# Kernel tuning notes

Measured on AMD Instinct MI355X. Metric: run time of the kernel, lower is better.

The kernel has to match this reference:

```python
import jax, jax.numpy as jnp
import numpy as np

B, T, Q, D = 8192, 65, 20, 100  # batch, tweet len, question len, 2*hidden_dim


def setup_inputs() -> dict:
    key = jax.random.key(0)
    kH, kU, k1, k2, k3 = jax.random.split(key, 5)
    # Ws params are a single normal row repeated across the length dim
    ws1 = jnp.tile(jax.random.normal(k1, (1, D), dtype=jnp.float32), (T, 1))
    ws2 = jnp.tile(jax.random.normal(k2, (1, D), dtype=jnp.float32), (Q, 1))
    ws3 = jnp.tile(jax.random.normal(k3, (1, D), dtype=jnp.float32), (T, 1))
    return {
        "H": jax.random.normal(kH, (B, T, D), dtype=jnp.float32),
        "U": jax.random.normal(kU, (B, Q, D), dtype=jnp.float32),
        "Ws1": ws1,
        "Ws2": ws2,
        "Ws3": ws3,
    }


def reference(H, U, Ws1, Ws2, Ws3):
    # H: [B,T,D], U: [B,Q,D]
    H1 = jnp.sum(H * Ws1, axis=2)[:, :, None]        # [B,T,1]
    U1 = jnp.sum(U * Ws2, axis=2)[:, None, :]        # [B,1,Q]
    HU = jnp.einsum('btd,bqd->btq', H * Ws3, U)      # [B,T,Q]
    S = H1 + U1 + HU                                 # [B,T,Q]
    at = jax.nn.softmax(S, axis=2)                   # attend tweet->question
    Util = jnp.einsum('btq,bqd->btd', at, U)         # [B,T,D]
    beta = jnp.max(S, axis=2)                        # [B,T]
    b = jax.nn.softmax(beta, axis=1)[:, :, None]     # [B,T,1]
    Htil = jnp.sum(b * H, axis=1)[:, None, :]        # [B,1,D] broadcast over T
    G = jnp.concatenate((H, Util, H * Util, H * Htil), axis=2)  # [B,T,4D]
    return G
```

## Files before the change

kernel.cpp:

```cpp
#include <hip/hip_runtime.h>
#include <math.h>

#define NB 8192
#define T 65
#define Q 20
#define D 100
#define D4 25
#define SP4 5

__global__ __launch_bounds__(256, 4) void attn_fused_kernel(
    const float* __restrict__ Hg,
    const float* __restrict__ Ug,
    const float* __restrict__ Ws1,
    const float* __restrict__ Ws2,
    const float* __restrict__ Ws3,
    float* __restrict__ Gg)
{
    __shared__ float4 sH4[T*D4];
    __shared__ float4 sU3e4[(Q+1)*D4];
    __shared__ float4 sS4[T*SP4];
    __shared__ float4 sHtilP[2][D4];
    __shared__ float4 sU1q4[5];
    __shared__ float  sScal[T];

    const int b    = blockIdx.x;
    const int tid  = threadIdx.x;
    const int wv   = tid >> 6;
    const int lane = tid & 63;
    const float4* Hb = (const float4*)(Hg + (size_t)b * (T*D));
    const float4* Ub = (const float4*)(Ug + (size_t)b * (Q*D));
    float* Gb = Gg + (size_t)b * (T*4*D);
    float4* Gb4 = (float4*)Gb;
    float* sSf = (float*)sS4;

    for (int i = tid; i < T*D4; i += 256) {
        const float4 h = Hb[i];
        sH4[i] = h;
        const int t = i / D4;
        const int g = i - t*D4;
        Gb4[t*100 + g] = h;
    }
    {
        const float4* w3g = (const float4*)Ws3;
        for (int i = tid; i < Q*D4; i += 256) {
            const float4 u = Ub[i];
            const int dd = i - (i/D4)*D4;
            const float4 w = w3g[dd];
            float4 v; v.x=u.x*w.x; v.y=u.y*w.y; v.z=u.z*w.z; v.w=u.w*w.w;
            sU3e4[i] = v;
        }
        if (tid < D4) sU3e4[Q*D4 + tid] = ((const float4*)Ws1)[tid];
    }
    __syncthreads();

    if (tid < 119) {
        const int tg = tid / 7;
        const int jg = tid - tg*7;
        int rb0 = ((tg*4 + 0) < T ? (tg*4 + 0) : T-1) * D4;
        int rb1 = ((tg*4 + 1) < T ? (tg*4 + 1) : T-1) * D4;
        int rb2 = ((tg*4 + 2) < T ? (tg*4 + 2) : T-1) * D4;
        int rb3 = ((tg*4 + 3) < T ? (tg*4 + 3) : T-1) * D4;
        float acc[4][3];
        #pragma unroll
        for (int i = 0; i < 4; ++i)
            #pragma unroll
            for (int k = 0; k < 3; ++k) acc[i][k] = 0.f;
        #pragma unroll 5
        for (int d4 = 0; d4 < D4; ++d4) {
            float4 h0 = sH4[rb0 + d4];
            float4 h1 = sH4[rb1 + d4];
            float4 h2 = sH4[rb2 + d4];
            float4 h3 = sH4[rb3 + d4];
            #pragma unroll
            for (int k = 0; k < 3; ++k) {
                const float4 w = sU3e4[(jg*3+k)*D4 + d4];
                acc[0][k] = fmaf(h0.x, w.x, acc[0][k]); acc[0][k] = fmaf(h0.y, w.y, acc[0][k]);
                acc[0][k] = fmaf(h0.z, w.z, acc[0][k]); acc[0][k] = fmaf(h0.w, w.w, acc[0][k]);
                acc[1][k] = fmaf(h1.x, w.x, acc[1][k]); acc[1][k] = fmaf(h1.y, w.y, acc[1][k]);
                acc[1][k] = fmaf(h1.z, w.z, acc[1][k]); acc[1][k] = fmaf(h1.w, w.w, acc[1][k]);
                acc[2][k] = fmaf(h2.x, w.x, acc[2][k]); acc[2][k] = fmaf(h2.y, w.y, acc[2][k]);
                acc[2][k] = fmaf(h2.z, w.z, acc[2][k]); acc[2][k] = fmaf(h2.w, w.w, acc[2][k]);
                acc[3][k] = fmaf(h3.x, w.x, acc[3][k]); acc[3][k] = fmaf(h3.y, w.y, acc[3][k]);
                acc[3][k] = fmaf(h3.z, w.z, acc[3][k]); acc[3][k] = fmaf(h3.w, w.w, acc[3][k]);
            }
        }
        #pragma unroll
        for (int i = 0; i < 4; ++i) {
            const int t = tg*4 + i;
            if (t < T) {
                #pragma unroll
                for (int k = 0; k < 3; ++k) {
                    const int cc = jg*3 + k;
                    if (cc < Q) sSf[t*Q + cc] = acc[i][k];
                    else        sScal[t] = acc[i][k];
                }
            }
        }
    } else if (tid >= 128 && tid < 128 + Q) {
        const int q = tid - 128;
        const float4* ur = Ub + q*D4;
        const float4* w2 = (const float4*)Ws2;
        float acc = 0.f;
        #pragma unroll 5
        for (int k = 0; k < D4; ++k) {
            const float4 u = ur[k], w = w2[k];
            acc = fmaf(u.x, w.x, acc); acc = fmaf(u.y, w.y, acc);
            acc = fmaf(u.z, w.z, acc); acc = fmaf(u.w, w.w, acc);
        }
        ((float*)sU1q4)[q] = acc;
    }
    __syncthreads();

    if (tid < T) {
        const int t = tid;
        float4 r[SP4];
        #pragma unroll
        for (int c = 0; c < SP4; ++c) {
            r[c] = sS4[t*SP4 + c];
            const float4 u1 = sU1q4[c];
            r[c].x += u1.x; r[c].y += u1.y; r[c].z += u1.z; r[c].w += u1.w;
        }
        float m = -1e30f;
        #pragma unroll
        for (int c = 0; c < SP4; ++c)
            m = fmaxf(m, fmaxf(fmaxf(r[c].x, r[c].y), fmaxf(r[c].z, r[c].w)));
        float s = 0.f;
        #pragma unroll
        for (int c = 0; c < SP4; ++c) {
            r[c].x = __expf(r[c].x - m); r[c].y = __expf(r[c].y - m);
            r[c].z = __expf(r[c].z - m); r[c].w = __expf(r[c].w - m);
            s += r[c].x + r[c].y + r[c].z + r[c].w;
        }
        const float inv = 1.f / s;
        #pragma unroll
        for (int c = 0; c < SP4; ++c) {
            r[c].x *= inv; r[c].y *= inv; r[c].z *= inv; r[c].w *= inv;
            sS4[t*SP4 + c] = r[c];
        }
        sScal[t] = sScal[t] + m;
    }
    __syncthreads();

    if (wv < 2) {
        const float v0 = sScal[lane];
        const float v1 = (lane == 0) ? sScal[64] : -1e30f;
        float mx = fmaxf(v0, v1);
        #pragma unroll
        for (int off = 32; off >= 1; off >>= 1)
            mx = fmaxf(mx, __shfl_xor(mx, off, 64));
        const float e0 = __expf(v0 - mx);
        const float e1 = (lane == 0) ? __expf(v1 - mx) : 0.f;
        float s = e0 + e1;
        #pragma unroll
        for (int off = 32; off >= 1; off >>= 1)
            s += __shfl_xor(s, off, 64);
        const float inv = 1.f / s;
        if (lane < D4) {
            float4 acc = {0.f, 0.f, 0.f, 0.f};
            for (int t = wv; t < T; t += 2) {
                const float bt = __expf(sScal[t] - mx) * inv;
                const float4 h = sH4[t*D4 + lane];
                acc.x = fmaf(bt, h.x, acc.x); acc.y = fmaf(bt, h.y, acc.y);
                acc.z = fmaf(bt, h.z, acc.z); acc.w = fmaf(bt, h.w, acc.w);
            }
            sHtilP[wv][lane] = acc;
        }
    }
    __syncthreads();

    {
        const int tsel = (lane < 50) ? (lane / 25) : 0;
        const int g    = (lane < 50) ? (lane - tsel*25) : (lane - 50);
        const bool act = (lane < 50);

        const float4 p0 = sHtilP[0][g], p1 = sHtilP[1][g];
        float4 htil;
        htil.x = p0.x+p1.x; htil.y = p0.y+p1.y;
        htil.z = p0.z+p1.z; htil.w = p0.w+p1.w;

        float4 u[Q];
        #pragma unroll
        for (int q = 0; q < Q; ++q) u[q] = Ub[q*D4 + g];

        #pragma unroll 1
        for (int pr = wv; pr < 33; pr += 4) {
            const int t   = pr*2 + tsel;
            const bool val = act && (t < T);
            const int tr  = val ? t : 0;

            float4 acc = {0.f, 0.f, 0.f, 0.f};
            #define QSTEP(av, comp, qq) { \
                acc.x = fmaf(av.comp, u[qq].x, acc.x); \
                acc.y = fmaf(av.comp, u[qq].y, acc.y); \
                acc.z = fmaf(av.comp, u[qq].z, acc.z); \
                acc.w = fmaf(av.comp, u[qq].w, acc.w); }
            {
                float4 a = sS4[tr*SP4 + 0];
                QSTEP(a,x,0)  QSTEP(a,y,1)  QSTEP(a,z,2)  QSTEP(a,w,3)
                a = sS4[tr*SP4 + 1];
                QSTEP(a,x,4)  QSTEP(a,y,5)  QSTEP(a,z,6)  QSTEP(a,w,7)
                a = sS4[tr*SP4 + 2];
                QSTEP(a,x,8)  QSTEP(a,y,9)  QSTEP(a,z,10) QSTEP(a,w,11)
                a = sS4[tr*SP4 + 3];
                QSTEP(a,x,12) QSTEP(a,y,13) QSTEP(a,z,14) QSTEP(a,w,15)
                a = sS4[tr*SP4 + 4];
                QSTEP(a,x,16) QSTEP(a,y,17) QSTEP(a,z,18) QSTEP(a,w,19)
            }
            #undef QSTEP

            const float4 hv = sH4[tr*D4 + g];
            if (val) {
                float4 hu, hh;
                hu.x = hv.x*acc.x;  hu.y = hv.y*acc.y;  hu.z = hv.z*acc.z;  hu.w = hv.w*acc.w;
                hh.x = hv.x*htil.x; hh.y = hv.y*htil.y; hh.z = hv.z*htil.z; hh.w = hv.w*htil.w;
                float4* base = (float4*)(Gb + (size_t)t*(4*D));
                base[D4 + g]   = acc;
                base[2*D4 + g] = hu;
                base[3*D4 + g] = hh;
            }
        }
    }
}

extern "C" void kernel_launch(void* const* d_in, const int* in_sizes, int n_in,
                              void* d_out, int out_size, void* d_ws, size_t ws_size,
                              hipStream_t stream) {
    const float* H   = (const float*)d_in[0];
    const float* U   = (const float*)d_in[1];
    const float* Ws1 = (const float*)d_in[2];
    const float* Ws2 = (const float*)d_in[3];
    const float* Ws3 = (const float*)d_in[4];
    float* G = (float*)d_out;
    hipLaunchKernelGGL(attn_fused_kernel, dim3(NB), dim3(256), 0, stream,
                       H, U, Ws1, Ws2, Ws3, G);
}
```

Measured before the change: 328.7 us.

## Make blocks persistent over 16 batches with async double-buffered H staging

Each 512-thread block now handles 16 consecutive batch items. It double-buffers H in LDS with global_load_lds, so the next item's H is fetched asynchronously while the current item's output is written. The next item's U*Ws3 and U*Ws2 terms are prefetched during the softmax phase, and H is copied to G from LDS in the output loop. This aims to hide global-load latency behind compute, at the cost of far fewer blocks (512 total), a larger LDS footprint and reliance on implicit completion of the async LDS loads at barriers.

```diff
diff --git a/kernel.cpp b/kernel.cpp
--- a/kernel.cpp
+++ b/kernel.cpp
@@ -7,8 +7,21 @@
 #define D 100
 #define D4 25
 #define SP4 5
-
-__global__ __launch_bounds__(256, 4) void attn_fused_kernel(
+#define NBPB 16
+#define HPAD 1632
+
+__device__ __forceinline__ void stage_H_async(float4* dst, const float4* src,
+                                              int wv, int lane, int tid) {
+    #pragma unroll 1
+    for (int i = wv; i < 25; i += 8) {
+        __builtin_amdgcn_global_load_lds(
+            (const __attribute__((address_space(1))) void*)(src + i*64 + lane),
+            (__attribute__((address_space(3))) void*)(dst + i*64), 16, 0, 0);
+    }
+    if (tid < 25) dst[1600 + tid] = src[1600 + tid];
+}
+
+__global__ __launch_bounds__(512, 4) void attn_fused_kernel(
     const float* __restrict__ Hg,
     const float* __restrict__ Ug,
     const float* __restrict__ Ws1,
@@ -16,209 +29,238 @@
     const float* __restrict__ Ws3,
     float* __restrict__ Gg)
 {
-    __shared__ float4 sH4[T*D4];
+    __shared__ float4 sH4[2][HPAD];
     __shared__ float4 sU3e4[(Q+1)*D4];
     __shared__ float4 sS4[T*SP4];
     __shared__ float4 sHtilP[2][D4];
-    __shared__ float4 sU1q4[5];
+    __shared__ float4 sU1q4[2][5];
     __shared__ float  sScal[T];
 
-    const int b    = blockIdx.x;
     const int tid  = threadIdx.x;
     const int wv   = tid >> 6;
     const int lane = tid & 63;
-    const float4* Hb = (const float4*)(Hg + (size_t)b * (T*D));
-    const float4* Ub = (const float4*)(Ug + (size_t)b * (Q*D));
-    float* Gb = Gg + (size_t)b * (T*4*D);
-    float4* Gb4 = (float4*)Gb;
+    const int b0   = blockIdx.x * NBPB;
+
+    const float4* Hg4 = (const float4*)Hg;
+    const float4* Ug4 = (const float4*)Ug;
+    const float4* w3g = (const float4*)Ws3;
+    const float4* w2g = (const float4*)Ws2;
     float* sSf = (float*)sS4;
 
-    for (int i = tid; i < T*D4; i += 256) {
-        const float4 h = Hb[i];
-        sH4[i] = h;
-        const int t = i / D4;
-        const int g = i - t*D4;
-        Gb4[t*100 + g] = h;
-    }
+    stage_H_async(sH4[0], Hg4 + (size_t)b0 * 1625, wv, lane, tid);
     {
-        const float4* w3g = (const float4*)Ws3;
-        for (int i = tid; i < Q*D4; i += 256) {
-            const float4 u = Ub[i];
+        const float4* Ub0 = Ug4 + (size_t)b0 * 500;
+        for (int i = tid; i < Q*D4; i += 512) {
+            const float4 u = Ub0[i];
             const int dd = i - (i/D4)*D4;
             const float4 w = w3g[dd];
             float4 v; v.x=u.x*w.x; v.y=u.y*w.y; v.z=u.z*w.z; v.w=u.w*w.w;
             sU3e4[i] = v;
         }
         if (tid < D4) sU3e4[Q*D4 + tid] = ((const float4*)Ws1)[tid];
+        if (tid >= 192 && tid < 192 + Q) {
+            const int q = tid - 192;
+            const float4* ur = Ub0 + q*D4;
+            float acc = 0.f;
+            #pragma unroll 5
+            for (int k = 0; k < D4; ++k) {
+                const float4 u = ur[k], w = w2g[k];
+                acc = fmaf(u.x, w.x, acc); acc = fmaf(u.y, w.y, acc);
+                acc = fmaf(u.z, w.z, acc); acc = fmaf(u.w, w.w, acc);
+            }
+            ((float*)sU1q4[0])[q] = acc;
+        }
     }
     __syncthreads();
 
-    if (tid < 119) {
-        const int tg = tid / 7;
-        const int jg = tid - tg*7;
-        int rb0 = ((tg*4 + 0) < T ? (tg*4 + 0) : T-1) * D4;
-        int rb1 = ((tg*4 + 1) < T ? (tg*4 + 1) : T-1) * D4;
-        int rb2 = ((tg*4 + 2) < T ? (tg*4 + 2) : T-1) * D4;
-        int rb3 = ((tg*4 + 3) < T ? (tg*4 + 3) : T-1) * D4;
-        float acc[4][3];
-        #pragma unroll
-        for (int i = 0; i < 4; ++i)
-            #pragma unroll
-            for (int k = 0; k < 3; ++k) acc[i][k] = 0.f;
-        #pragma unroll 5
-        for (int d4 = 0; d4 < D4; ++d4) {
-            float4 h0 = sH4[rb0 + d4];
-            float4 h1 = sH4[rb1 + d4];
-            float4 h2 = sH4[rb2 + d4];
-            float4 h3 = sH4[rb3 + d4];
-            #pragma unroll
-            for (int k = 0; k < 3; ++k) {
-                const float4 w = sU3e4[(jg*3+k)*D4 + d4];
-                acc[0][k] = fmaf(h0.x, w.x, acc[0][k]); acc[0][k] = fmaf(h0.y, w.y, acc[0][k]);
-                acc[0][k] = fmaf(h0.z, w.z, acc[0][k]); acc[0][k] = fmaf(h0.w, w.w, acc[0][k]);
-                acc[1][k] = fmaf(h1.x, w.x, acc[1][k]); acc[1][k] = fmaf(h1.y, w.y, acc[1][k]);
-                acc[1][k] = fmaf(h1.z, w.z, acc[1][k]); acc[1][k] = fmaf(h1.w, w.w, acc[1][k]);
-                acc[2][k] = fmaf(h2.x, w.x, acc[2][k]); acc[2][k] = fmaf(h2.y, w.y, acc[2][k]);
-                acc[2][k] = fmaf(h2.z, w.z, acc[2][k]); acc[2][k] = fmaf(h2.w, w.w, acc[2][k]);
-                acc[3][k] = fmaf(h3.x, w.x, acc[3][k]); acc[3][k] = fmaf(h3.y, w.y, acc[3][k]);
-                acc[3][k] = fmaf(h3.z, w.z, acc[3][k]); acc[3][k] = fmaf(h3.w, w.w, acc[3][k]);
-            }
-        }
-        #pragma unroll
-        for (int i = 0; i < 4; ++i) {
-            const int t = tg*4 + i;
-            if (t < T) {
+    #pragma unroll 1
+    for (int j = 0; j < NBPB; ++j) {
+        const int b   = b0 + j;
+        const int cur = j & 1;
+        const int nxt = cur ^ 1;
+        float4* bufc = sH4[cur];
+        const float4* Ub  = Ug4 + (size_t)b * 500;
+        float* Gb = Gg + (size_t)b * 26000;
+        const bool more = (j + 1 < NBPB);
+
+        if (tid < 119) {
+            const int tg = tid / 7;
+            const int jg = tid - tg*7;
+            int rb0 = ((tg*4 + 0) < T ? (tg*4 + 0) : T-1) * D4;
+            int rb1 = ((tg*4 + 1) < T ? (tg*4 + 1) : T-1) * D4;
+            int rb2 = ((tg*4 + 2) < T ? (tg*4 + 2) : T-1) * D4;
+            int rb3 = ((tg*4 + 3) < T ? (tg*4 + 3) : T-1) * D4;
+            float acc[4][3];
+            #pragma unroll
+            for (int i = 0; i < 4; ++i)
+                #pragma unroll
+                for (int k = 0; k < 3; ++k) acc[i][k] = 0.f;
+            #pragma unroll 5
+            for (int d4 = 0; d4 < D4; ++d4) {
+                float4 h0 = bufc[rb0 + d4];
+                float4 h1 = bufc[rb1 + d4];
+                float4 h2 = bufc[rb2 + d4];
+                float4 h3 = bufc[rb3 + d4];
                 #pragma unroll
                 for (int k = 0; k < 3; ++k) {
-                    const int cc = jg*3 + k;
-                    if (cc < Q) sSf[t*Q + cc] = acc[i][k];
-                    else        sScal[t] = acc[i][k];
-                }
-            }
-        }
-    } else if (tid >= 128 && tid < 128 + Q) {
-        const int q = tid - 128;
-        const float4* ur = Ub + q*D4;
-        const float4* w2 = (const float4*)Ws2;
-        float acc = 0.f;
-        #pragma unroll 5
-        for (int k = 0; k < D4; ++k) {
-            const float4 u = ur[k], w = w2[k];
-            acc = fmaf(u.x, w.x, acc); acc = fmaf(u.y, w.y, acc);
-            acc = fmaf(u.z, w.z, acc); acc = fmaf(u.w, w.w, acc);
-        }
-        ((float*)sU1q4)[q] = acc;
-    }
-    __syncthreads();
-
-    if (tid < T) {
-        const int t = tid;
-        float4 r[SP4];
-        #pragma unroll
-        for (int c = 0; c < SP4; ++c) {
-            r[c] = sS4[t*SP4 + c];
-            const float4 u1 = sU1q4[c];
-            r[c].x += u1.x; r[c].y += u1.y; r[c].z += u1.z; r[c].w += u1.w;
-        }
-        float m = -1e30f;
-        #pragma unroll
-        for (int c = 0; c < SP4; ++c)
-            m = fmaxf(m, fmaxf(fmaxf(r[c].x, r[c].y), fmaxf(r[c].z, r[c].w)));
-        float s = 0.f;
-        #pragma unroll
-        for (int c = 0; c < SP4; ++c) {
-            r[c].x = __expf(r[c].x - m); r[c].y = __expf(r[c].y - m);
-            r[c].z = __expf(r[c].z - m); r[c].w = __expf(r[c].w - m);
-            s += r[c].x + r[c].y + r[c].z + r[c].w;
-        }
-        const float inv = 1.f / s;
-        #pragma unroll
-        for (int c = 0; c < SP4; ++c) {
-            r[c].x *= inv; r[c].y *= inv; r[c].z *= inv; r[c].w *= inv;
-            sS4[t*SP4 + c] = r[c];
-        }
-        sScal[t] = sScal[t] + m;
-    }
-    __syncthreads();
-
-    if (wv < 2) {
-        const float v0 = sScal[lane];
-        const float v1 = (lane == 0) ? sScal[64] : -1e30f;
-        float mx = fmaxf(v0, v1);
-        #pragma unroll
-        for (int off = 32; off >= 1; off >>= 1)
-            mx = fmaxf(mx, __shfl_xor(mx, off, 64));
-        const float e0 = __expf(v0 - mx);
-        const float e1 = (lane == 0) ? __expf(v1 - mx) : 0.f;
-        float s = e0 + e1;
-        #pragma unroll
-        for (int off = 32; off >= 1; off >>= 1)
-            s += __shfl_xor(s, off, 64);
-        const float inv = 1.f / s;
-        if (lane < D4) {
-            float4 acc = {0.f, 0.f, 0.f, 0.f};
-            for (int t = wv; t < T; t += 2) {
-                const float bt = __expf(sScal[t] - mx) * inv;
-                const float4 h = sH4[t*D4 + lane];
-                acc.x = fmaf(bt, h.x, acc.x); acc.y = fmaf(bt, h.y, acc.y);
-                acc.z = fmaf(bt, h.z, acc.z); acc.w = fmaf(bt, h.w, acc.w);
-            }
-            sHtilP[wv][lane] = acc;
-        }
-    }
-    __syncthreads();
-
-    {
-        const int tsel = (lane < 50) ? (lane / 25) : 0;
-        const int g    = (lane < 50) ? (lane - tsel*25) : (lane - 50);
-        const bool act = (lane < 50);
-
-        const float4 p0 = sHtilP[0][g], p1 = sHtilP[1][g];
-        float4 htil;
-        htil.x = p0.x+p1.x; htil.y = p0.y+p1.y;
-        htil.z = p0.z+p1.z; htil.w = p0.w+p1.w;
-
-        float4 u[Q];
-        #pragma unroll
-        for (int q = 0; q < Q; ++q) u[q] = Ub[q*D4 + g];
-
-        #pragma unroll 1
-        for (int pr = wv; pr < 33; pr += 4) {
-            const int t   = pr*2 + tsel;
-            const bool val = act && (t < T);
-            const int tr  = val ? t : 0;
-
-            float4 acc = {0.f, 0.f, 0.f, 0.f};
-            #define QSTEP(av, comp, qq) { \
-                acc.x = fmaf(av.comp, u[qq].x, acc.x); \
-                acc.y = fmaf(av.comp, u[qq].y, acc.y); \
-                acc.z = fmaf(av.comp, u[qq].z, acc.z); \
-                acc.w = fmaf(av.comp, u[qq].w, acc.w); }
-            {
-                float4 a = sS4[tr*SP4 + 0];
-                QSTEP(a,x,0)  QSTEP(a,y,1)  QSTEP(a,z,2)  QSTEP(a,w,3)
-                a = sS4[tr*SP4 + 1];
-                QSTEP(a,x,4)  QSTEP(a,y,5)  QSTEP(a,z,6)  QSTEP(a,w,7)
-                a = sS4[tr*SP4 + 2];
-                QSTEP(a,x,8)  QSTEP(a,y,9)  QSTEP(a,z,10) QSTEP(a,w,11)
-                a = sS4[tr*SP4 + 3];
-                QSTEP(a,x,12) QSTEP(a,y,13) QSTEP(a,z,14) QSTEP(a,w,15)
-                a = sS4[tr*SP4 + 4];
-                QSTEP(a,x,16) QSTEP(a,y,17) QSTEP(a,z,18) QSTEP(a,w,19)
-            }
-            #undef QSTEP
-
-            const float4 hv = sH4[tr*D4 + g];
-            if (val) {
-                float4 hu, hh;
-                hu.x = hv.x*acc.x;  hu.y = hv.y*acc.y;  hu.z = hv.z*acc.z;  hu.w = hv.w*acc.w;
-                hh.x = hv.x*htil.x; hh.y = hv.y*htil.y; hh.z = hv.z*htil.z; hh.w = hv.w*htil.w;
-                float4* base = (float4*)(Gb + (size_t)t*(4*D));
-                base[D4 + g]   = acc;
-                base[2*D4 + g] = hu;
-                base[3*D4 + g] = hh;
-            }
-        }
+                    const float4 w = sU3e4[(jg*3+k)*D4 + d4];
+                    acc[0][k] = fmaf(h0.x, w.x, acc[0][k]); acc[0][k] = fmaf(h0.y, w.y, acc[0][k]);
+                    acc[0][k] = fmaf(h0.z, w.z, acc[0][k]); acc[0][k] = fmaf(h0.w, w.w, acc[0][k]);
+                    acc[1][k] = fmaf(h1.x, w.x, acc[1][k]); acc[1][k] = fmaf(h1.y, w.y, acc[1][k]);
+                    acc[1][k] = fmaf(h1.z, w.z, acc[1][k]); acc[1][k] = fmaf(h1.w, w.w, acc[1][k]);
+                    acc[2][k] = fmaf(h2.x, w.x, acc[2][k]); acc[2][k] = fmaf(h2.y, w.y, acc[2][k]);
+                    acc[2][k] = fmaf(h2.z, w.z, acc[2][k]); acc[2][k] = fmaf(h2.w, w.w, acc[2][k]);
+                    acc[3][k] = fmaf(h3.x, w.x, acc[3][k]); acc[3][k] = fmaf(h3.y, w.y, acc[3][k]);
+                    acc[3][k] = fmaf(h3.z, w.z, acc[3][k]); acc[3][k] = fmaf(h3.w, w.w, acc[3][k]);
+                }
+            }
+            #pragma unroll
+            for (int i = 0; i < 4; ++i) {
+                const int t = tg*4 + i;
+                if (t < T) {
+                    #pragma unroll
+                    for (int k = 0; k < 3; ++k) {
+                        const int cc = jg*3 + k;
+                        if (cc < Q) sSf[t*Q + cc] = acc[i][k];
+                        else        sScal[t] = acc[i][k];
+                    }
+                }
+            }
+        }
+        __syncthreads();
+
+        if (tid < T) {
+            const int t = tid;
+            float4 r[SP4];
+            #pragma unroll
+            for (int c = 0; c < SP4; ++c) {
+                r[c] = sS4[t*SP4 + c];
+                const float4 u1 = sU1q4[cur][c];
+                r[c].x += u1.x; r[c].y += u1.y; r[c].z += u1.z; r[c].w += u1.w;
+            }
+            float m = -1e30f;
+            #pragma unroll
+            for (int c = 0; c < SP4; ++c)
+                m = fmaxf(m, fmaxf(fmaxf(r[c].x, r[c].y), fmaxf(r[c].z, r[c].w)));
+            float s = 0.f;
+            #pragma unroll
+            for (int c = 0; c < SP4; ++c) {
+                r[c].x = __expf(r[c].x - m); r[c].y = __expf(r[c].y - m);
+                r[c].z = __expf(r[c].z - m); r[c].w = __expf(r[c].w - m);
+                s += r[c].x + r[c].y + r[c].z + r[c].w;
+            }
+            const float inv = 1.f / s;
+            #pragma unroll
+            for (int c = 0; c < SP4; ++c) {
+                r[c].x *= inv; r[c].y *= inv; r[c].z *= inv; r[c].w *= inv;
+                sS4[t*SP4 + c] = r[c];
+            }
+            sScal[t] = sScal[t] + m;
+        } else if (more && tid >= 192 && tid < 192 + Q) {
+            const int q = tid - 192;
+            const float4* ur = Ug4 + (size_t)(b+1) * 500 + q*D4;
+            float acc = 0.f;
+            #pragma unroll 5
+            for (int k = 0; k < D4; ++k) {
+                const float4 u = ur[k], w = w2g[k];
+                acc = fmaf(u.x, w.x, acc); acc = fmaf(u.y, w.y, acc);
+                acc = fmaf(u.z, w.z, acc); acc = fmaf(u.w, w.w, acc);
+            }
+            ((float*)sU1q4[nxt])[q] = acc;
+        } else if (more && tid >= 256) {
+            const float4* Ub1 = Ug4 + (size_t)(b+1) * 500;
+            for (int i = tid - 256; i < Q*D4; i += 256) {
+                const float4 u = Ub1[i];
+                const int dd = i - (i/D4)*D4;
+                const float4 w = w3g[dd];
+                float4 v; v.x=u.x*w.x; v.y=u.y*w.y; v.z=u.z*w.z; v.w=u.w*w.w;
+                sU3e4[i] = v;
+            }
+        }
+        __syncthreads();
+
+        if (wv < 2) {
+            const float v0 = sScal[lane];
+            const float v1 = (lane == 0) ? sScal[64] : -1e30f;
+            float mx = fmaxf(v0, v1);
+            #pragma unroll
+            for (int off = 32; off >= 1; off >>= 1)
+                mx = fmaxf(mx, __shfl_xor(mx, off, 64));
+            const float e0 = __expf(v0 - mx);
+            const float e1 = (lane == 0) ? __expf(v1 - mx) : 0.f;
+            float s = e0 + e1;
+            #pragma unroll
+            for (int off = 32; off >= 1; off >>= 1)
+                s += __shfl_xor(s, off, 64);
+            const float inv = 1.f / s;
+            if (lane < D4) {
+                float4 acc = {0.f, 0.f, 0.f, 0.f};
+                for (int t = wv; t < T; t += 2) {
+                    const float bt = __expf(sScal[t] - mx) * inv;
+                    const float4 h = bufc[t*D4 + lane];
+                    acc.x = fmaf(bt, h.x, acc.x); acc.y = fmaf(bt, h.y, acc.y);
+                    acc.z = fmaf(bt, h.z, acc.z); acc.w = fmaf(bt, h.w, acc.w);
+                }
+                sHtilP[wv][lane] = acc;
+            }
+        }
+        __syncthreads();
+
+        if (more) stage_H_async(sH4[nxt], Hg4 + (size_t)(b+1) * 1625, wv, lane, tid);
+        {
+            const int tsel = (lane < 50) ? (lane / 25) : 0;
+            const int g    = (lane < 50) ? (lane - tsel*25) : (lane - 50);
+            const bool act = (lane < 50);
+
+            const float4 p0 = sHtilP[0][g], p1 = sHtilP[1][g];
+            float4 htil;
+            htil.x = p0.x+p1.x; htil.y = p0.y+p1.y;
+            htil.z = p0.z+p1.z; htil.w = p0.w+p1.w;
+
+            float4 u[Q];
+            #pragma unroll
+            for (int q = 0; q < Q; ++q) u[q] = Ub[q*D4 + g];
+
+            #pragma unroll 1
+            for (int pr = wv; pr < 33; pr += 8) {
+                const int t   = pr*2 + tsel;
+                const bool val = act && (t < T);
+                const int tr  = val ? t : 0;
+
+                float4 acc = {0.f, 0.f, 0.f, 0.f};
+                #define QSTEP(av, comp, qq) { \
+                    acc.x = fmaf(av.comp, u[qq].x, acc.x); \
+                    acc.y = fmaf(av.comp, u[qq].y, acc.y); \
+                    acc.z = fmaf(av.comp, u[qq].z, acc.z); \
+                    acc.w = fmaf(av.comp, u[qq].w, acc.w); }
+                {
+                    float4 a = sS4[tr*SP4 + 0];
+                    QSTEP(a,x,0)  QSTEP(a,y,1)  QSTEP(a,z,2)  QSTEP(a,w,3)
+                    a = sS4[tr*SP4 + 1];
+                    QSTEP(a,x,4)  QSTEP(a,y,5)  QSTEP(a,z,6)  QSTEP(a,w,7)
+                    a = sS4[tr*SP4 + 2];
+                    QSTEP(a,x,8)  QSTEP(a,y,9)  QSTEP(a,z,10) QSTEP(a,w,11)
+                    a = sS4[tr*SP4 + 3];
+                    QSTEP(a,x,12) QSTEP(a,y,13) QSTEP(a,z,14) QSTEP(a,w,15)
+                    a = sS4[tr*SP4 + 4];
+                    QSTEP(a,x,16) QSTEP(a,y,17) QSTEP(a,z,18) QSTEP(a,w,19)
+                }
+                #undef QSTEP
+
+                const float4 hv = bufc[tr*D4 + g];
+                if (val) {
+                    float4 hu, hh;
+                    hu.x = hv.x*acc.x;  hu.y = hv.y*acc.y;  hu.z = hv.z*acc.z;  hu.w = hv.w*acc.w;
+                    hh.x = hv.x*htil.x; hh.y = hv.y*htil.y; hh.z = hv.z*htil.z; hh.w = hv.w*htil.w;
+                    float4* base = (float4*)(Gb + (size_t)t*(4*D));
+                    base[g]        = hv;
+                    base[D4 + g]   = acc;
+                    base[2*D4 + g] = hu;
+                    base[3*D4 + g] = hh;
+                }
+            }
+        }
+        __syncthreads();
     }
 }
 
@@ -231,6 +273,6 @@
     const float* Ws2 = (const float*)d_in[3];
     const float* Ws3 = (const float*)d_in[4];
     float* G = (float*)d_out;
-    hipLaunchKernelGGL(attn_fused_kernel, dim3(NB), dim3(256), 0, stream,
+    hipLaunchKernelGGL(attn_fused_kernel, dim3(NB / NBPB), dim3(512), 0, stream,
                        H, U, Ws1, Ws2, Ws3, G);
 }
```

After: 392.1 us. 19.3% more time.
